# Kernel tuning notes

Hardware: AMD Instinct MI355X
Metric: run time of the kernel (lower is better)

## Reference

```python
import jax, jax.numpy as jnp
import numpy as np

OUT_FEATURES = 8192
IN_FEATURES = 8192
BATCH = 512


def setup_inputs() -> dict:
    key = jax.random.key(0)
    k_x, k_w, k_s = jax.random.split(key, 3)
    x = jax.random.normal(k_x, (BATCH, IN_FEATURES), dtype=jnp.float32)
    # packed int4 weights: each int holds two nibbles (values 0..255)
    packed_weight = jax.random.randint(k_w, (OUT_FEATURES, IN_FEATURES // 2), 0, 256, dtype=jnp.int32)
    # per-output-row scale (positive, as produced by abs-max quantization)
    scale = jax.random.uniform(k_s, (OUT_FEATURES, 1), dtype=jnp.float32) * 0.02 + 1e-4
    return {"x": x, "packed_weight": packed_weight, "scale": scale}


def reference(x, packed_weight, scale):
    # Unpack two 4-bit values per byte: high nibble first (matches torch loop:
    # col i <- packed >> 4 & 15, col i+1 <- packed & 15), then subtract zero-point 8.
    hi = (packed_weight >> 4) & 15
    lo = packed_weight & 15
    q = jnp.stack([hi, lo], axis=-1).reshape(OUT_FEATURES, IN_FEATURES) - 8  # [out, in] int
    w = q.astype(scale.dtype) * scale  # dequantized weight [out, in]
    # linear: y = x @ W^T
    return jnp.einsum('bi,oi->bo', x, w)
```

## Files before the change

### kernel.cpp

```cpp
#include <hip/hip_runtime.h>
#include <cstdint>
#include <cstddef>

#define IN_F 8192
#define OUT_F 8192
#define BATCH 512
#define KSPLIT 4
#define KSLICE (IN_F / KSPLIT)
#define BK 64
#define NIT (KSLICE / BK)

typedef __bf16 bf16x8 __attribute__((ext_vector_type(8)));
typedef float floatx4 __attribute__((ext_vector_type(4)));

__device__ __forceinline__ ushort f2bf(float f) {
  uint32_t u = __float_as_uint(f);
  u += 0x7FFFu + ((u >> 16) & 1u);
  return (ushort)(u >> 16);
}

__device__ __forceinline__ uint32_t perm(uint32_t a, uint32_t b, uint32_t s) {
  return __builtin_amdgcn_perm(a, b, s);
}

__device__ __forceinline__ uint32_t low4(const int4 p) {
  uint32_t qa = perm((uint32_t)p.y, (uint32_t)p.x, 0x00000400u);
  uint32_t qb = perm((uint32_t)p.w, (uint32_t)p.z, 0x00000400u);
  return perm(qb, qa, 0x05040100u);
}

__device__ __forceinline__ bf16x8 unpack8(uint32_t u) {
  uint32_t hi = (u >> 4) & 0x0F0F0F0Fu;
  uint32_t lo = u & 0x0F0F0F0Fu;
  uint32_t hl0 = perm(hi, lo, 0x01050004u);
  uint32_t hl1 = perm(hi, lo, 0x03070206u);
  const uint32_t c43 = 0x43434343u;
  uint4 d;
  d.x = perm(hl0, c43, 0x00050004u);
  d.y = perm(hl0, c43, 0x00070006u);
  d.z = perm(hl1, c43, 0x00050004u);
  d.w = perm(hl1, c43, 0x00070006u);
  union { uint4 u4; bf16x8 v; } cv;
  cv.u4 = d;
  return cv.v;
}

__device__ __forceinline__ void async_copy16(const void* g, void* l) {
  __builtin_amdgcn_global_load_lds((__attribute__((address_space(1))) void*)(g),
                                   (__attribute__((address_space(3))) void*)(l),
                                   16, 0, 0);
}

__global__ __launch_bounds__(256) void cvt_rowsum(const float* __restrict__ x,
                                                  ushort* __restrict__ xb,
                                                  float* __restrict__ rowsum) {
  const int b = blockIdx.x;
  const int t = threadIdx.x;
  const float4* xr = (const float4*)(x + (size_t)b * IN_F);
  ushort4* xo = (ushort4*)(xb + (size_t)b * IN_F);
  float s[4] = {0.f, 0.f, 0.f, 0.f};
#pragma unroll
  for (int i = 0; i < 8; ++i) {
    float4 v = xr[i * 256 + t];
    ushort4 o;
    o.x = f2bf(v.x); o.y = f2bf(v.y); o.z = f2bf(v.z); o.w = f2bf(v.w);
    xo[i * 256 + t] = o;
    s[i >> 1] += __uint_as_float((uint32_t)o.x << 16) + __uint_as_float((uint32_t)o.y << 16)
               + __uint_as_float((uint32_t)o.z << 16) + __uint_as_float((uint32_t)o.w << 16);
  }
  __shared__ float red[4][4];
  const int lane = t & 63, wid = t >> 6;
#pragma unroll
  for (int j = 0; j < 4; ++j) {
    float v = s[j];
#pragma unroll
    for (int off = 32; off >= 1; off >>= 1) v += __shfl_down(v, off, 64);
    if (lane == 0) red[wid][j] = v;
  }
  __syncthreads();
  if (t < 4) rowsum[t * BATCH + b] = red[0][t] + red[1][t] + red[2][t] + red[3][t];
}

__global__ __launch_bounds__(256, 3) void qgemm(const ushort* __restrict__ xb,
                                                const int* __restrict__ pw,
                                                const float* __restrict__ scale,
                                                const float* __restrict__ rowsum,
                                                float* __restrict__ out) {
  __shared__ __align__(16) char Asm[2][16384];
  __shared__ __align__(16) char Bsm[2][4096];

  const int tid = threadIdx.x;
  const int lane = tid & 63;
  const int w = tid >> 6;
  const int wm = w & 1, wn = w >> 1;
  const int lr = lane & 15, lq = lane >> 4;

  const int n0 = blockIdx.x * 128;
  const int m0 = blockIdx.y * 128;
  const int ks = blockIdx.z;

  const int aRow = w * 32 + (lane >> 3);
  const int ac = ((lane & 7) ^ ((lane >> 3) & 7)) * 16;
  const char* aG = (const char*)xb + (size_t)(m0 + aRow) * (IN_F * 2) + ks * (KSLICE * 2) + ac;

  const int rB = tid >> 1, hB = tid & 1;
  const char* bG = (const char*)pw + (size_t)(n0 + rB) * (IN_F * 2) + ks * (KSLICE * 2) + hB * 64;

  floatx4 acc[4][4] = {};

#pragma unroll
  for (int j = 0; j < 4; ++j)
    async_copy16(aG + (size_t)j * 8 * (IN_F * 2), Asm[0] + w * 4096 + j * 1024);
  int4 p0 = *(const int4*)(bG);
  int4 p1 = *(const int4*)(bG + 16);
  int4 p2 = *(const int4*)(bG + 32);
  int4 p3 = *(const int4*)(bG + 48);

#pragma unroll 2
  for (int it = 0; it < NIT; ++it) {
    const int c = it & 1;
    int4 dd;
    dd.x = low4(p0); dd.y = low4(p1); dd.z = low4(p2); dd.w = low4(p3);
    *(int4*)(Bsm[c] + rB * 32 + hB * 16) = dd;
    __syncthreads();
    if (it + 1 < NIT) {
      const char* ag = aG + (it + 1) * (BK * 2);
#pragma unroll
      for (int j = 0; j < 4; ++j)
        async_copy16(ag + (size_t)j * 8 * (IN_F * 2), Asm[c ^ 1] + w * 4096 + j * 1024);
      const char* bg = bG + (it + 1) * (BK * 2);
      p0 = *(const int4*)(bg);
      p1 = *(const int4*)(bg + 16);
      p2 = *(const int4*)(bg + 32);
      p3 = *(const int4*)(bg + 48);
    }
    const char* aBase = Asm[c] + (wm * 64 + lr) * 128;
    const char* bBase = Bsm[c] + (wn * 64 + lr) * 32 + lq * 4;
#pragma unroll
    for (int kk = 0; kk < 2; ++kk) {
      const int pc = ((kk * 4 + lq) ^ (lr & 7)) * 16;
      bf16x8 av[4], bv[4];
#pragma unroll
      for (int mi = 0; mi < 4; ++mi) av[mi] = *(const bf16x8*)(aBase + mi * 2048 + pc);
#pragma unroll
      for (int ni = 0; ni < 4; ++ni) bv[ni] = unpack8(*(const uint32_t*)(bBase + ni * 512 + kk * 16));
#pragma unroll
      for (int mi = 0; mi < 4; ++mi)
#pragma unroll
        for (int ni = 0; ni < 4; ++ni)
          acc[mi][ni] = __builtin_amdgcn_mfma_f32_16x16x32_bf16(av[mi], bv[ni],
                                                                acc[mi][ni], 0, 0, 0);
    }
  }

  const int om = m0 + wm * 64 + lq * 4;
  const int on = n0 + wn * 64 + lr;
  float scv[4];
#pragma unroll
  for (int ni = 0; ni < 4; ++ni) scv[ni] = scale[on + ni * 16];
  float rsv[4][4];
#pragma unroll
  for (int mi = 0; mi < 4; ++mi)
#pragma unroll
    for (int rr = 0; rr < 4; ++rr)
      rsv[mi][rr] = rowsum[ks * BATCH + om + mi * 16 + rr];

#pragma unroll
  for (int mi = 0; mi < 4; ++mi)
#pragma unroll
    for (int ni = 0; ni < 4; ++ni) {
      const float s = scv[ni];
      float* op = out + (size_t)(om + mi * 16) * OUT_F + (on + ni * 16);
#pragma unroll
      for (int rr = 0; rr < 4; ++rr)
        atomicAdd(op + (size_t)rr * OUT_F, s * (acc[mi][ni][rr] - 136.f * rsv[mi][rr]));
    }
}

extern "C" void kernel_launch(void* const* d_in, const int* in_sizes, int n_in,
                              void* d_out, int out_size, void* d_ws, size_t ws_size,
                              hipStream_t stream) {
  const float* x = (const float*)d_in[0];
  const int* pw = (const int*)d_in[1];
  const float* scale = (const float*)d_in[2];
  float* out = (float*)d_out;

  ushort* xb = (ushort*)d_ws;
  float* rowsum = (float*)((char*)d_ws + (size_t)BATCH * IN_F * sizeof(ushort));

  cvt_rowsum<<<BATCH, 256, 0, stream>>>(x, xb, rowsum);
  hipMemsetAsync(out, 0, (size_t)out_size * sizeof(float), stream);
  dim3 grid(OUT_F / 128, BATCH / 128, KSPLIT);
  qgemm<<<grid, 256, 0, stream>>>(xb, pw, scale, rowsum, out);
}
```

Before: 320.9 us.

## Pre-compact int32 nibble weights into packed bytes and async-load B to LDS

```diff
diff --git a/kernel.cpp b/kernel.cpp
--- a/kernel.cpp
+++ b/kernel.cpp
@@ -81,8 +81,23 @@
   if (t < 4) rowsum[t * BATCH + b] = red[0][t] + red[1][t] + red[2][t] + red[3][t];
 }
 
-__global__ __launch_bounds__(256, 3) void qgemm(const ushort* __restrict__ xb,
-                                                const int* __restrict__ pw,
+#define NPKT (OUT_F * (IN_F / 2) / 16)
+__global__ __launch_bounds__(256) void bcompact(const int* __restrict__ pw,
+                                                int4* __restrict__ bc) {
+  const int g = blockIdx.x * 256 + threadIdx.x;
+#pragma unroll
+  for (int i = 0; i < 4; ++i) {
+    const size_t p = (size_t)g + (size_t)i * 524288;
+    const int4* src = (const int4*)(pw + p * 16);
+    int4 a = src[0], b = src[1], c = src[2], d = src[3];
+    int4 o;
+    o.x = (int)low4(a); o.y = (int)low4(b); o.z = (int)low4(c); o.w = (int)low4(d);
+    bc[p] = o;
+  }
+}
+
+__global__ __launch_bounds__(256, 4) void qgemm(const ushort* __restrict__ xb,
+                                                const char* __restrict__ bc,
                                                 const float* __restrict__ scale,
                                                 const float* __restrict__ rowsum,
                                                 float* __restrict__ out) {
@@ -102,48 +117,43 @@
   const int aRow = w * 32 + (lane >> 3);
   const int ac = ((lane & 7) ^ ((lane >> 3) & 7)) * 16;
   const char* aG = (const char*)xb + (size_t)(m0 + aRow) * (IN_F * 2) + ks * (KSLICE * 2) + ac;
-
-  const int rB = tid >> 1, hB = tid & 1;
-  const char* bG = (const char*)pw + (size_t)(n0 + rB) * (IN_F * 2) + ks * (KSLICE * 2) + hB * 64;
+  char* aL = Asm[0] + w * 4096;
+
+  const char* bG = bc + (size_t)(n0 + (tid >> 1)) * (IN_F / 2) + ks * (KSLICE / 2) + (tid & 1) * 16;
+  char* bL = Bsm[0] + w * 1024;
 
   floatx4 acc[4][4] = {};
 
+  const char* aBase = Asm[0] + (wm * 64 + lr) * 128;
+  const char* bBase = Bsm[0] + (wn * 64 + lr) * 32 + lq * 4;
+
 #pragma unroll
   for (int j = 0; j < 4; ++j)
-    async_copy16(aG + (size_t)j * 8 * (IN_F * 2), Asm[0] + w * 4096 + j * 1024);
-  int4 p0 = *(const int4*)(bG);
-  int4 p1 = *(const int4*)(bG + 16);
-  int4 p2 = *(const int4*)(bG + 32);
-  int4 p3 = *(const int4*)(bG + 48);
+    async_copy16(aG + (size_t)j * 8 * (IN_F * 2), aL + j * 1024);
+  async_copy16(bG, bL);
 
 #pragma unroll 2
   for (int it = 0; it < NIT; ++it) {
     const int c = it & 1;
-    int4 dd;
-    dd.x = low4(p0); dd.y = low4(p1); dd.z = low4(p2); dd.w = low4(p3);
-    *(int4*)(Bsm[c] + rB * 32 + hB * 16) = dd;
     __syncthreads();
     if (it + 1 < NIT) {
+      const int nc = c ^ 1;
       const char* ag = aG + (it + 1) * (BK * 2);
 #pragma unroll
       for (int j = 0; j < 4; ++j)
-        async_copy16(ag + (size_t)j * 8 * (IN_F * 2), Asm[c ^ 1] + w * 4096 + j * 1024);
-      const char* bg = bG + (it + 1) * (BK * 2);
-      p0 = *(const int4*)(bg);
-      p1 = *(const int4*)(bg + 16);
-      p2 = *(const int4*)(bg + 32);
-      p3 = *(const int4*)(bg + 48);
+        async_copy16(ag + (size_t)j * 8 * (IN_F * 2), aL + nc * 16384 + j * 1024);
+      async_copy16(bG + (it + 1) * (BK / 2), bL + nc * 4096);
     }
-    const char* aBase = Asm[c] + (wm * 64 + lr) * 128;
-    const char* bBase = Bsm[c] + (wn * 64 + lr) * 32 + lq * 4;
 #pragma unroll
     for (int kk = 0; kk < 2; ++kk) {
       const int pc = ((kk * 4 + lq) ^ (lr & 7)) * 16;
       bf16x8 av[4], bv[4];
 #pragma unroll
-      for (int mi = 0; mi < 4; ++mi) av[mi] = *(const bf16x8*)(aBase + mi * 2048 + pc);
-#pragma unroll
-      for (int ni = 0; ni < 4; ++ni) bv[ni] = unpack8(*(const uint32_t*)(bBase + ni * 512 + kk * 16));
+      for (int mi = 0; mi < 4; ++mi)
+        av[mi] = *(const bf16x8*)(aBase + c * 16384 + mi * 2048 + pc);
+#pragma unroll
+      for (int ni = 0; ni < 4; ++ni)
+        bv[ni] = unpack8(*(const uint32_t*)(bBase + c * 4096 + ni * 512 + kk * 16));
 #pragma unroll
       for (int mi = 0; mi < 4; ++mi)
 #pragma unroll
@@ -186,10 +196,12 @@
   float* out = (float*)d_out;
 
   ushort* xb = (ushort*)d_ws;
-  float* rowsum = (float*)((char*)d_ws + (size_t)BATCH * IN_F * sizeof(ushort));
+  float* rowsum = (float*)((char*)d_ws + (8u << 20));
+  char* bc = (char*)d_ws + (16u << 20);
 
   cvt_rowsum<<<BATCH, 256, 0, stream>>>(x, xb, rowsum);
+  bcompact<<<2048, 256, 0, stream>>>(pw, (int4*)bc);
   hipMemsetAsync(out, 0, (size_t)out_size * sizeof(float), stream);
   dim3 grid(OUT_F / 128, BATCH / 128, KSPLIT);
-  qgemm<<<grid, 256, 0, stream>>>(xb, pw, scale, rowsum, out);
-}
+  qgemm<<<grid, 256, 0, stream>>>(xb, bc, scale, rowsum, out);
+}
```

Result: faster. 312.6 us (-2.6%).
